# Kernel tuning notes

Measured on AMD Instinct MI355X. Metric: run time of the kernel, lower is better.

Reference implementation:

```python
import jax, jax.numpy as jnp
import numpy as np

jax.config.update("jax_enable_x64", True)

NUM_SQRTM = 6      # PSDMatrixLogm(num_sqrtm=6, ...)
PADE_ORDER = 8     # PSDMatrixLogm(..., pade_order=8)
_n, _w = np.polynomial.legendre.leggauss(PADE_ORDER)
PADE_NODES = tuple((_n + 1.0) / 2.0)   # Gauss-Legendre nodes mapped to [0,1]
PADE_WEIGHTS = tuple(_w / 2.0)
NUM_STATE = 500000
NOISE_RATE = 0.233


def setup_inputs() -> dict:
    key = jax.random.key(0)
    k1, k2 = jax.random.split(key)
    # torch code: np_rng.uniform(-1, 1, size=...) for both parameters (float64)
    theta_coeff = jax.random.uniform(k1, (NUM_STATE,), jnp.float64, -1.0, 1.0)
    theta_state = jax.random.uniform(k2, (NUM_STATE, 2, 2), jnp.float64, -1.0, 1.0)
    g = NOISE_RATE
    # amplitude damping Kraus ops: K0 = [[1,0],[0,sqrt(1-g)]], K1 = [[0,sqrt(g)],[0,0]]
    kop = jnp.array([[[1.0, 0.0], [0.0, float(np.sqrt(1.0 - g))]],
                     [[0.0, float(np.sqrt(g))], [0.0, 0.0]]], dtype=jnp.float64)
    return {"theta_coeff": theta_coeff, "theta_state": theta_state, "kop": kop}


def _sqrtm_psd(A):
    # Hermitian PSD matrix square root (batched over leading dims)
    w, v = jnp.linalg.eigh(A)
    w = jnp.clip(w, 0.0, None)
    return (v * jnp.sqrt(w)[..., None, :]) @ jnp.conj(jnp.swapaxes(v, -1, -2))


def psd_logm(A):
    # inverse scaling-and-squaring logm: NUM_SQRTM successive square roots,
    # then order-PADE_ORDER Gauss-Legendre Pade approximant of log(I + X)
    for _ in range(NUM_SQRTM):
        A = _sqrtm_psd(A)
    eye = jnp.eye(A.shape[-1], dtype=A.dtype)
    X = A - eye
    ret = jnp.zeros_like(A)
    for w, t in zip(PADE_WEIGHTS, PADE_NODES):
        ret = ret + w * jnp.linalg.solve(eye + t * X, X)
    return ret * float(2 ** NUM_SQRTM)


def _vne(rho):
    # von Neumann entropy: -Re Tr(rho^dag log(rho)), batched over leading dims
    log_rho = psd_logm(rho)
    return -jnp.real(jnp.einsum('...ij,...ij->...', jnp.conj(rho), log_rho))


def reference(theta_coeff, theta_state, kop):
    kop = kop.astype(jnp.complex128)               # (num_kraus=2, dim_out=2, dim_in=2)
    t = jax.nn.softplus(theta_coeff)
    coeff = t / t.sum()                            # convex mixture weights (N,)
    nrm = jnp.sqrt(jnp.sum(theta_state * theta_state, axis=(1, 2), keepdims=True))
    s = theta_state / nrm                          # unit-norm (N, dim_in, 2)
    state = (s[:, :, 0] + 1j * s[:, :, 1]).astype(jnp.complex128)  # (N, dim_in)
    rho = (state.T * coeff) @ jnp.conj(state)      # (dim_in, dim_in) average input state
    # contract0: channel applied to rho -> (dim_out, dim_out)
    rho_out = jnp.einsum('aoc,apd,cd->op', kop, jnp.conj(kop), rho)
    # contract1: channel applied to each pure state -> (N, dim_out, dim_out)
    phi = jnp.einsum('aoc,nc->nao', kop, state)
    sigma = jnp.einsum('nao,nap->nop', phi, jnp.conj(phi))
    # negative Holevo quantity
    return -(_vne(rho_out) - jnp.dot(coeff, _vne(sigma)))
```

## Files before the change

### kernel.cpp

```cpp
#include <hip/hip_runtime.h>
#include <hip/hip_bf16.h>
#include <stdint.h>

#define BLOCK 256
#define NBLK  512

#define G_NOISE 0.233

#define GL_T0 0.019855071751231856
#define GL_T1 0.10166676129318663
#define GL_T2 0.23723379504183550
#define GL_T3 0.40828267875217510
#define GL_T4 0.59171732124782490
#define GL_T5 0.76276620495816449
#define GL_T6 0.89833323870681337
#define GL_T7 0.98014492824876811
#define GL_W0 0.05061426814518813
#define GL_W1 0.11119051722668723
#define GL_W2 0.15685332293894364
#define GL_W3 0.18134107081135099

__device__ __forceinline__ float F_pade_fast(float lam) {
    if (!(lam > 0.0f)) return 0.0f;
    const float TJ[8] = {(float)GL_T0,(float)GL_T1,(float)GL_T2,(float)GL_T3,
                         (float)GL_T4,(float)GL_T5,(float)GL_T6,(float)GL_T7};
    const float WJ[8] = {(float)GL_W0,(float)GL_W1,(float)GL_W2,(float)GL_W3,
                         (float)GL_W3,(float)GL_W2,(float)GL_W1,(float)GL_W0};
    float x = __expf(__logf(lam) * 0.015625f) - 1.0f;
    float s = 0.0f;
#pragma unroll
    for (int j = 0; j < 8; ++j)
        s += __fdividef(WJ[j] * x, fmaf(TJ[j], x, 1.0f));
    return 64.0f * lam * s;
}

__device__ __forceinline__ double F_pade_d(double lam) {
    if (!(lam > 0.0)) return 0.0;
    const double TJ[8] = {GL_T0,GL_T1,GL_T2,GL_T3,GL_T4,GL_T5,GL_T6,GL_T7};
    const double WJ[8] = {GL_W0,GL_W1,GL_W2,GL_W3,GL_W3,GL_W2,GL_W1,GL_W0};
    double x = expm1(log(lam) * 0.015625);
    double s = 0.0;
#pragma unroll
    for (int j = 0; j < 8; ++j)
        s += WJ[j] * x / fma(TJ[j], x, 1.0);
    return 64.0 * lam * s;
}

__device__ __forceinline__ void sample_terms(float c, float4 s, float gg,
                                             bool valid, float out[5]) {
    float t = __logf(1.0f + __expf(c));
    if (!valid) t = 0.0f;
    float n2 = fmaf(s.x, s.x, fmaf(s.y, s.y, fmaf(s.z, s.z, s.w * s.w)));
    float inv = __fdividef(1.0f, n2);
    float q  = (s.z * s.z + s.w * s.w) * inv;
    float cr = (s.x * s.z + s.y * s.w) * inv;
    float ci = (s.y * s.z - s.x * s.w) * inv;
    float det = gg * q * q;
    float disc = sqrtf(0.25f - det);
    float lp = 0.5f + disc;
    float lm = __fdividef(det, lp);
    float E = -(F_pade_fast(lp) + F_pade_fast(lm));
    out[0] = t; out[1] = t * q; out[2] = t * cr; out[3] = t * ci; out[4] = t * E;
}

__global__ __launch_bounds__(BLOCK) void reduce_kernel(
    const float* __restrict__ coeff, const float4* __restrict__ state,
    double* __restrict__ partial, int N)
{
    const float gg = (float)(G_NOISE * (1.0 - G_NOISE));
    const int tid = blockIdx.x * BLOCK + threadIdx.x;
    const int T = NBLK * BLOCK;

    const int i1 = tid + T, i2 = tid + 2 * T, i3 = tid + 3 * T;
    const bool v3 = (i3 < N);
    float  c0 = coeff[tid],  c1 = coeff[i1],  c2 = coeff[i2];
    float4 s0 = state[tid],  s1 = state[i1],  s2 = state[i2];
    float  c3 = v3 ? coeff[i3] : 0.0f;
    float4 s3 = v3 ? state[i3] : make_float4(1.f, 0.f, 0.f, 0.f);

    float r0[5], r1[5], r2[5], r3[5];
    sample_terms(c0, s0, gg, true, r0);
    sample_terms(c1, s1, gg, true, r1);
    sample_terms(c2, s2, gg, true, r2);
    sample_terms(c3, s3, gg, v3,   r3);

    double acc[5];
#pragma unroll
    for (int k = 0; k < 5; ++k)
        acc[k] = ((double)r0[k] + (double)r1[k]) + ((double)r2[k] + (double)r3[k]);

    for (int i = tid + 4 * T; i < N; i += T) {
        float rr[5];
        sample_terms(coeff[i], state[i], gg, true, rr);
#pragma unroll
        for (int k = 0; k < 5; ++k) acc[k] += (double)rr[k];
    }

    __shared__ double smem[BLOCK / 64][5];
    const int lane = threadIdx.x & 63, wave = threadIdx.x >> 6;
#pragma unroll
    for (int k = 0; k < 5; ++k) {
        double v = acc[k];
        for (int o = 32; o > 0; o >>= 1) v += __shfl_down(v, o, 64);
        if (lane == 0) smem[wave][k] = v;
    }
    __syncthreads();
    if (threadIdx.x == 0) {
#pragma unroll
        for (int k = 0; k < 5; ++k)
            partial[blockIdx.x * 5 + k] =
                smem[0][k] + smem[1][k] + smem[2][k] + smem[3][k];
    }
}

__global__ __launch_bounds__(BLOCK) void final_kernel(
    const double* __restrict__ partial, float* __restrict__ out)
{
    const int t = threadIdx.x;
    double v[5];
#pragma unroll
    for (int k = 0; k < 5; ++k)
        v[k] = partial[t * 5 + k] + partial[(t + BLOCK) * 5 + k];

    __shared__ double smem[BLOCK / 64][5];
    const int lane = t & 63, wave = t >> 6;
#pragma unroll
    for (int k = 0; k < 5; ++k) {
        double x = v[k];
        for (int o = 32; o > 0; o >>= 1) x += __shfl_down(x, o, 64);
        if (lane == 0) smem[wave][k] = x;
    }
    __syncthreads();
    if (t == 0) {
        double T  = smem[0][0] + smem[1][0] + smem[2][0] + smem[3][0];
        double B  = smem[0][1] + smem[1][1] + smem[2][1] + smem[3][1];
        double Cr = smem[0][2] + smem[1][2] + smem[2][2] + smem[3][2];
        double Ci = smem[0][3] + smem[1][3] + smem[2][3] + smem[3][3];
        double D  = smem[0][4] + smem[1][4] + smem[2][4] + smem[3][4];

        const double b2 = G_NOISE;
        const double a2 = 1.0 - G_NOISE;
        double r11 = B / T;
        double r00 = 1.0 - r11;
        double c2  = (Cr * Cr + Ci * Ci) / (T * T);
        double det = (r00 + b2 * r11) * (a2 * r11) - a2 * c2;
        double disc = 0.25 - det;
        disc = disc > 0.0 ? sqrt(disc) : 0.0;
        double lp = 0.5 + disc;
        double lm = lp > 0.0 ? det / lp : 0.0;
        double S_out = -(F_pade_d(lp) + F_pade_d(lm));
        double res = -S_out + D / T;

        out[0] = (float)res;
    }
}

extern "C" void kernel_launch(void* const* d_in, const int* in_sizes, int n_in,
                              void* d_out, int out_size, void* d_ws, size_t ws_size,
                              hipStream_t stream) {
    const float*  coeff = (const float*)d_in[0];
    const float4* state = (const float4*)d_in[1];
    const int N = in_sizes[0];
    double* partial = (double*)d_ws;

    reduce_kernel<<<NBLK, BLOCK, 0, stream>>>(coeff, state, partial, N);
    final_kernel<<<1, BLOCK, 0, stream>>>(partial, (float*)d_out);
}
```

Before: 16.91 us.

## Fuse final reduction into main kernel via last-block atomic counter

Merges the two-kernel reduction into a single kernel. Each block writes its partial sums to padded slots and increments a global atomic counter, and the last block to arrive performs the final reduction and the scalar entropy computation. This removes the second kernel launch and its dependency gap. In exchange it adds a memset on the stream to reset the counter, plus atomic traffic and a tail in which one block works alone.

```diff
diff --git a/kernel.cpp b/kernel.cpp
--- a/kernel.cpp
+++ b/kernel.cpp
@@ -4,6 +4,7 @@
 
 #define BLOCK 256
 #define NBLK  512
+#define SLOT  8
 
 #define G_NOISE 0.233
 
@@ -63,9 +64,10 @@
     out[0] = t; out[1] = t * q; out[2] = t * cr; out[3] = t * ci; out[4] = t * E;
 }
 
-__global__ __launch_bounds__(BLOCK) void reduce_kernel(
+__global__ __launch_bounds__(BLOCK) void fused_kernel(
     const float* __restrict__ coeff, const float4* __restrict__ state,
-    double* __restrict__ partial, int N)
+    double* __restrict__ ws, unsigned long long* __restrict__ counter,
+    float* __restrict__ out, int N)
 {
     const float gg = (float)(G_NOISE * (1.0 - G_NOISE));
     const int tid = blockIdx.x * BLOCK + threadIdx.x;
@@ -97,6 +99,7 @@
     }
 
     __shared__ double smem[BLOCK / 64][5];
+    __shared__ int last_flag;
     const int lane = threadIdx.x & 63, wave = threadIdx.x >> 6;
 #pragma unroll
     for (int k = 0; k < 5; ++k) {
@@ -106,24 +109,29 @@
     }
     __syncthreads();
     if (threadIdx.x == 0) {
+        double* slot = ws + (size_t)blockIdx.x * SLOT;
 #pragma unroll
-        for (int k = 0; k < 5; ++k)
-            partial[blockIdx.x * 5 + k] =
-                smem[0][k] + smem[1][k] + smem[2][k] + smem[3][k];
+        for (int k = 0; k < 5; ++k) {
+            double v = smem[0][k] + smem[1][k] + smem[2][k] + smem[3][k];
+            __hip_atomic_store(&slot[k], v, __ATOMIC_RELAXED, __HIP_MEMORY_SCOPE_AGENT);
+        }
+        unsigned long long old = __hip_atomic_fetch_add(
+            counter, 1ull, __ATOMIC_ACQ_REL, __HIP_MEMORY_SCOPE_AGENT);
+        last_flag = (old == (unsigned long long)(NBLK - 1)) ? 1 : 0;
     }
-}
+    __syncthreads();
+    if (!last_flag) return;
 
-__global__ __launch_bounds__(BLOCK) void final_kernel(
-    const double* __restrict__ partial, float* __restrict__ out)
-{
     const int t = threadIdx.x;
     double v[5];
 #pragma unroll
     for (int k = 0; k < 5; ++k)
-        v[k] = partial[t * 5 + k] + partial[(t + BLOCK) * 5 + k];
+        v[k] = __hip_atomic_load(ws + (size_t)t * SLOT + k,
+                                 __ATOMIC_RELAXED, __HIP_MEMORY_SCOPE_AGENT)
+             + __hip_atomic_load(ws + (size_t)(t + BLOCK) * SLOT + k,
+                                 __ATOMIC_RELAXED, __HIP_MEMORY_SCOPE_AGENT);
 
-    __shared__ double smem[BLOCK / 64][5];
-    const int lane = t & 63, wave = t >> 6;
+    __syncthreads();
 #pragma unroll
     for (int k = 0; k < 5; ++k) {
         double x = v[k];
@@ -132,24 +140,24 @@
     }
     __syncthreads();
     if (t == 0) {
-        double T  = smem[0][0] + smem[1][0] + smem[2][0] + smem[3][0];
-        double B  = smem[0][1] + smem[1][1] + smem[2][1] + smem[3][1];
-        double Cr = smem[0][2] + smem[1][2] + smem[2][2] + smem[3][2];
-        double Ci = smem[0][3] + smem[1][3] + smem[2][3] + smem[3][3];
-        double D  = smem[0][4] + smem[1][4] + smem[2][4] + smem[3][4];
+        double T_  = smem[0][0] + smem[1][0] + smem[2][0] + smem[3][0];
+        double B   = smem[0][1] + smem[1][1] + smem[2][1] + smem[3][1];
+        double Cr  = smem[0][2] + smem[1][2] + smem[2][2] + smem[3][2];
+        double Ci  = smem[0][3] + smem[1][3] + smem[2][3] + smem[3][3];
+        double D   = smem[0][4] + smem[1][4] + smem[2][4] + smem[3][4];
 
         const double b2 = G_NOISE;
         const double a2 = 1.0 - G_NOISE;
-        double r11 = B / T;
+        double r11 = B / T_;
         double r00 = 1.0 - r11;
-        double c2  = (Cr * Cr + Ci * Ci) / (T * T);
+        double c2  = (Cr * Cr + Ci * Ci) / (T_ * T_);
         double det = (r00 + b2 * r11) * (a2 * r11) - a2 * c2;
         double disc = 0.25 - det;
         disc = disc > 0.0 ? sqrt(disc) : 0.0;
         double lp = 0.5 + disc;
         double lm = lp > 0.0 ? det / lp : 0.0;
         double S_out = -(F_pade_d(lp) + F_pade_d(lm));
-        double res = -S_out + D / T;
+        double res = -S_out + D / T_;
 
         out[0] = (float)res;
     }
@@ -161,8 +169,11 @@
     const float*  coeff = (const float*)d_in[0];
     const float4* state = (const float4*)d_in[1];
     const int N = in_sizes[0];
-    double* partial = (double*)d_ws;
+    double* ws = (double*)d_ws;
+    unsigned long long* counter =
+        (unsigned long long*)((char*)d_ws + (size_t)NBLK * SLOT * sizeof(double));
 
-    reduce_kernel<<<NBLK, BLOCK, 0, stream>>>(coeff, state, partial, N);
-    final_kernel<<<1, BLOCK, 0, stream>>>(partial, (float*)d_out);
+    hipMemsetAsync(counter, 0, sizeof(unsigned long long), stream);
+    fused_kernel<<<NBLK, BLOCK, 0, stream>>>(coeff, state, ws, counter,
+                                             (float*)d_out, N);
 }
```

After: 28.31 us. 67.4% more time.
